# Kernel optimization log

Hardware: AMD Instinct MI355X
Metric: run time of the kernel (lower is better)

Reference implementation:

```python
import jax, jax.numpy as jnp
import numpy as np

STIM_KER_LEN = 50  # length of causal stimulus kernel
K_BASIS = 2        # number of exponential basis functions in history kernel


def setup_inputs() -> dict:
    key = jax.random.key(0)
    T, NTR = 8192, 1024
    k0, k1, k2 = jax.random.split(key, 3)
    t = jnp.arange(T, dtype=jnp.float32)                    # uniform grid, dt = 1.0
    stim = jax.random.normal(k0, (T,), jnp.float32)
    rand = jax.random.uniform(k1, (T, NTR), jnp.float32)    # per-step uniforms (torch.rand in loop)
    # learned parameters
    bias = jnp.array([-4.0], jnp.float32)                   # nn.Parameter bias
    k_stim = jax.random.normal(k2, (STIM_KER_LEN,), jnp.float32) * 0.1  # stim kernel weights
    hist_w = jnp.array([-5.0, 1.0], jnp.float32)            # exponential basis coefficients
    hist_tau = jnp.array([5.0, 20.0], jnp.float32)          # exponential basis time constants
    return dict(t=t, stim=stim, rand=rand, bias=bias, k_stim=k_stim,
                hist_w=hist_w, hist_tau=hist_tau)


def reference(t, stim, rand, bias, k_stim, hist_w, hist_tau):
    dt = t[1] - t[0]
    T = t.shape[0]
    ntr = rand.shape[1]
    # stim_kernel(stim, dt): causal convolution scaled by dt, then shift_tensor(..., 1, fill=0)
    stim_conv = jnp.convolve(stim, k_stim)[:T] * dt                       # (T,)
    stim_conv = jnp.concatenate([jnp.zeros((1,), stim.dtype), stim_conv[:-1]])
    # history kernel: ker(s) = sum_k hist_w[k] * exp(-s / hist_tau[k]), evaluated from 0
    # one step after each spike -> linear recurrence on per-basis state s (K, ntr).
    decay = jnp.exp(-dt / hist_tau)                                        # (K,)

    def step(s, inp):
        sc_j, r_j = inp                       # scalar, (ntr,)
        hist_j = jnp.sum(s, axis=0)           # (ntr,) == hist_conv[j]
        loglam_j = bias[0] + sc_j + hist_j    # (ntr,)
        p_spk = 1.0 - jnp.exp(-jnp.exp(loglam_j) * dt)
        spk_j = p_spk > r_j                   # (ntr,) bool
        s_new = decay[:, None] * s + hist_w[:, None] * spk_j.astype(s.dtype)
        return s_new, (loglam_j, spk_j)

    s0 = jnp.zeros((hist_w.shape[0], ntr), jnp.float32)
    _, (log_lam, mask_spikes) = jax.lax.scan(step, s0, (stim_conv, rand))
    return log_lam, mask_spikes
```

## Files before the change

### kernel.cpp

```cpp
#include <hip/hip_runtime.h>
#include <math.h>

#define T_LEN 8192
#define NTRIALS 1024
#define TN ((size_t)T_LEN * NTRIALS)
#define KLEN 50
#define CHUNK 256
#define NCHUNK (T_LEN / CHUNK)
#define FARW 256
#define NEARW 256
#define WARM (FARW + NEARW)
#define PF 16
#define BAND 1e-4f

__global__ void prep_basc_kernel(const float* __restrict__ t,
                                 const float* __restrict__ stim,
                                 const float* __restrict__ bias,
                                 const float* __restrict__ k_stim,
                                 const float* __restrict__ hist_w,
                                 const float* __restrict__ hist_tau,
                                 double* __restrict__ dparams,
                                 double* __restrict__ basc,
                                 float* __restrict__ bascf) {
  int j = blockIdx.x * blockDim.x + threadIdx.x;
  if (j >= T_LEN) return;
  double dt = (double)t[1] - (double)t[0];
  if (j == 0) {
    dparams[0] = exp(-dt / (double)hist_tau[0]);
    dparams[1] = exp(-dt / (double)hist_tau[1]);
    dparams[2] = (double)hist_w[0];
    dparams[3] = (double)hist_w[1];
    dparams[4] = dt;
    basc[0] = (double)bias[0];
    bascf[0] = (float)(double)bias[0];
    return;
  }
  int n = j - 1;
  int mmax = n < (KLEN - 1) ? n : (KLEN - 1);
  double acc = 0.0;
  for (int m = 0; m <= mmax; ++m)
    acc += (double)k_stim[m] * (double)stim[n - m];
  double v = (double)bias[0] + dt * acc;
  basc[j] = v;
  bascf[j] = (float)v;
}

__global__ void prep_thr32_kernel(const float* __restrict__ rnd,
                                  const float* __restrict__ bascf,
                                  const double* __restrict__ dparams,
                                  float* __restrict__ thr32) {
  size_t m = ((size_t)blockIdx.x * blockDim.x + threadIdx.x) * 4;
  float dtf = (float)dparams[4];
  float4 r4 = *reinterpret_cast<const float4*>(rnd + m);
  float b = bascf[m >> 10];
  float4 o;
  o.x = logf(-log1pf(-r4.x) / dtf) - b;
  o.y = logf(-log1pf(-r4.y) / dtf) - b;
  o.z = logf(-log1pf(-r4.z) / dtf) - b;
  o.w = logf(-log1pf(-r4.w) / dtf) - b;
  *reinterpret_cast<float4*>(thr32 + m) = o;
}

__device__ __noinline__ bool decide64(const float* __restrict__ rnd,
                                      const double* __restrict__ basc,
                                      double dt, int j, int i, double h) {
  double r = (double)rnd[(size_t)j * NTRIALS + i];
  double t = log(-log1p(-r) / dt) - basc[j];
  return h > t;
}

__global__ __launch_bounds__(64, 1) void spec_scan2_kernel(
    const float* __restrict__ thr, const float* __restrict__ rnd,
    const double* __restrict__ basc, const float* __restrict__ bascf,
    const double* __restrict__ dparams, float* __restrict__ out) {
  const int tid = threadIdx.x;
  const int tb  = blockIdx.x & 15;
  const int c   = blockIdx.x >> 4;
  const int i   = tb * 64 + tid;
  const double d0 = dparams[0], d1 = dparams[1];
  const double w0 = dparams[2], w1 = dparams[3];
  const double dt = dparams[4];
  const float d0f = (float)d0, d1f = (float)d1;
  const float w0f = (float)w0, w1f = (float)w1;

  const int jstart = c * CHUNK;
  const int nw    = jstart < WARM ? jstart : WARM;
  const int jw    = jstart - nw;
  const int nearn = nw < NEARW ? nw : NEARW;
  const int farn  = nw - nearn;
  const int j1    = jw + farn;

  const float* __restrict__ p = thr + i;
  float bufA[PF], bufB[PF];
#pragma unroll
  for (int k = 0; k < PF; ++k) bufA[k] = p[(size_t)(jw + k) * NTRIALS];
  __builtin_amdgcn_sched_barrier(0);

  float a0 = 0.0f, a1 = 0.0f;
  for (int q = 0; q < farn; q += 2 * PF) {
    const int j0 = jw + q;
#pragma unroll
    for (int k = 0; k < PF; ++k) bufB[k] = p[(size_t)(j0 + PF + k) * NTRIALS];
    __builtin_amdgcn_sched_barrier(0);
#pragma unroll
    for (int k = 0; k < PF; ++k) {
      float h = a0 + a1;
      bool s = h > bufA[k];
      a0 = fmaf(d0f, a0, s ? w0f : 0.0f);
      a1 = fmaf(d1f, a1, s ? w1f : 0.0f);
    }
    __builtin_amdgcn_sched_barrier(0);
#pragma unroll
    for (int k = 0; k < PF; ++k) bufA[k] = p[(size_t)(j0 + 2 * PF + k) * NTRIALS];
    __builtin_amdgcn_sched_barrier(0);
#pragma unroll
    for (int k = 0; k < PF; ++k) {
      float h = a0 + a1;
      bool s = h > bufB[k];
      a0 = fmaf(d0f, a0, s ? w0f : 0.0f);
      a1 = fmaf(d1f, a1, s ? w1f : 0.0f);
    }
    __builtin_amdgcn_sched_barrier(0);
  }

  double s0 = (double)a0, s1 = (double)a1;
  for (int q = 0; q < nearn; q += 2 * PF) {
    const int j0 = j1 + q;
#pragma unroll
    for (int k = 0; k < PF; ++k) bufB[k] = p[(size_t)(j0 + PF + k) * NTRIALS];
    __builtin_amdgcn_sched_barrier(0);
#pragma unroll
    for (int k = 0; k < PF; ++k) {
      double h = s0 + s1;
      float d = (float)h - bufA[k];
      bool s = d > 0.0f;
      if (__builtin_expect(fabsf(d) < BAND, 0))
        s = decide64(rnd, basc, dt, j0 + k, i, h);
      s0 = fma(d0, s0, s ? w0 : 0.0);
      s1 = fma(d1, s1, s ? w1 : 0.0);
    }
    __builtin_amdgcn_sched_barrier(0);
#pragma unroll
    for (int k = 0; k < PF; ++k) bufA[k] = p[(size_t)(j0 + 2 * PF + k) * NTRIALS];
    __builtin_amdgcn_sched_barrier(0);
#pragma unroll
    for (int k = 0; k < PF; ++k) {
      double h = s0 + s1;
      float d = (float)h - bufB[k];
      bool s = d > 0.0f;
      if (__builtin_expect(fabsf(d) < BAND, 0))
        s = decide64(rnd, basc, dt, j0 + PF + k, i, h);
      s0 = fma(d0, s0, s ? w0 : 0.0);
      s1 = fma(d1, s1, s ? w1 : 0.0);
    }
    __builtin_amdgcn_sched_barrier(0);
  }

  float* __restrict__ po_ll = out + (size_t)jstart * NTRIALS + i;
  float* __restrict__ po_mk = po_ll + TN;
  for (int q = 0; q < CHUNK; q += 2 * PF) {
    const int j0 = jstart + q;
#pragma unroll
    for (int k = 0; k < PF; ++k) bufB[k] = p[(size_t)(j0 + PF + k) * NTRIALS];
    __builtin_amdgcn_sched_barrier(0);
#pragma unroll
    for (int k = 0; k < PF; ++k) {
      double h = s0 + s1;
      float d = (float)h - bufA[k];
      bool s = d > 0.0f;
      if (__builtin_expect(fabsf(d) < BAND, 0))
        s = decide64(rnd, basc, dt, j0 + k, i, h);
      po_ll[(size_t)(q + k) * NTRIALS] = (float)h + bascf[j0 + k];
      po_mk[(size_t)(q + k) * NTRIALS] = s ? 1.0f : 0.0f;
      s0 = fma(d0, s0, s ? w0 : 0.0);
      s1 = fma(d1, s1, s ? w1 : 0.0);
    }
    __builtin_amdgcn_sched_barrier(0);
    if (q + 2 * PF < CHUNK) {
#pragma unroll
      for (int k = 0; k < PF; ++k)
        bufA[k] = p[(size_t)(j0 + 2 * PF + k) * NTRIALS];
    }
    __builtin_amdgcn_sched_barrier(0);
#pragma unroll
    for (int k = 0; k < PF; ++k) {
      double h = s0 + s1;
      float d = (float)h - bufB[k];
      bool s = d > 0.0f;
      if (__builtin_expect(fabsf(d) < BAND, 0))
        s = decide64(rnd, basc, dt, j0 + PF + k, i, h);
      po_ll[(size_t)(q + PF + k) * NTRIALS] = (float)h + bascf[j0 + PF + k];
      po_mk[(size_t)(q + PF + k) * NTRIALS] = s ? 1.0f : 0.0f;
      s0 = fma(d0, s0, s ? w0 : 0.0);
      s1 = fma(d1, s1, s ? w1 : 0.0);
    }
    __builtin_amdgcn_sched_barrier(0);
  }
}

__global__ __launch_bounds__(64, 1) void glm_scan_inline_kernel(
    const float* __restrict__ rnd, const double* __restrict__ basc,
    const double* __restrict__ dparams, float* __restrict__ out) {
  const int i = blockIdx.x * 64 + threadIdx.x;
  const double d0 = dparams[0], d1 = dparams[1];
  const double w0 = dparams[2], w1 = dparams[3];
  const double dt = dparams[4];
  double s0 = 0.0, s1 = 0.0;
  float* __restrict__ out_ll = out;
  float* __restrict__ out_mk = out + TN;
  for (int j = 0; j < T_LEN; ++j) {
    double r = (double)rnd[(size_t)j * NTRIALS + i];
    double th = log(-log1p(-r) / dt) - basc[j];
    double hist = s0 + s1;
    bool spk = hist > th;
    out_ll[(size_t)j * NTRIALS + i] = (float)(basc[j] + hist);
    out_mk[(size_t)j * NTRIALS + i] = spk ? 1.0f : 0.0f;
    s0 = fma(d0, s0, spk ? w0 : 0.0);
    s1 = fma(d1, s1, spk ? w1 : 0.0);
  }
}

extern "C" void kernel_launch(void* const* d_in, const int* in_sizes, int n_in,
                              void* d_out, int out_size, void* d_ws, size_t ws_size,
                              hipStream_t stream) {
  const float* t        = (const float*)d_in[0];
  const float* stim     = (const float*)d_in[1];
  const float* rnd      = (const float*)d_in[2];
  const float* bias     = (const float*)d_in[3];
  const float* k_stim   = (const float*)d_in[4];
  const float* hist_w   = (const float*)d_in[5];
  const float* hist_tau = (const float*)d_in[6];
  float* out = (float*)d_out;

  char* ws = (char*)d_ws;
  const size_t off_bascf = 64;
  const size_t off_basc  = off_bascf + (size_t)T_LEN * 4;
  const size_t off_thr   = off_basc + (size_t)T_LEN * 8;
  const size_t need_full = off_thr + TN * 4;
  const size_t need_min  = off_thr;

  double* dparams = (double*)ws;
  float*  bascf   = (float*)(ws + off_bascf);
  double* basc    = (double*)(ws + off_basc);
  float*  thr32   = (float*)(ws + off_thr);

  prep_basc_kernel<<<(T_LEN + 255) / 256, 256, 0, stream>>>(
      t, stim, bias, k_stim, hist_w, hist_tau, dparams, basc, bascf);

  if (ws_size >= need_full) {
    prep_thr32_kernel<<<(int)(TN / 4 / 256), 256, 0, stream>>>(
        rnd, bascf, dparams, thr32);
    spec_scan2_kernel<<<NCHUNK * 16, 64, 0, stream>>>(
        thr32, rnd, basc, bascf, dparams, out);
  } else if (ws_size >= need_min) {
    glm_scan_inline_kernel<<<NTRIALS / 64, 64, 0, stream>>>(rnd, basc, dparams, out);
  }
}
```

Measured before the change: 96.34 us.

## Fuse threshold computation into chunked scan, halve chunk size, deepen prefetch

Removes the separate prep kernel that turned the uniforms into log-space thresholds, which wrote and then reread a full T×NTR float array. The scan now computes each threshold inline from the raw random value, using a precomputed log(dt). Chunk size is halved to 128 to launch twice as many blocks, and the prefetch depth is doubled to 32. The cost is more transcendental work inside the scan, including on the warm-up steps, which are repeated for every chunk, so redundant warm-up work relative to useful output grows.

```diff
diff --git a/kernel.cpp b/kernel.cpp
--- a/kernel.cpp
+++ b/kernel.cpp
@@ -5,12 +5,12 @@
 #define NTRIALS 1024
 #define TN ((size_t)T_LEN * NTRIALS)
 #define KLEN 50
-#define CHUNK 256
+#define CHUNK 128
 #define NCHUNK (T_LEN / CHUNK)
 #define FARW 256
 #define NEARW 256
 #define WARM (FARW + NEARW)
-#define PF 16
+#define PF 32
 #define BAND 1e-4f
 
 __global__ void prep_basc_kernel(const float* __restrict__ t,
@@ -31,6 +31,7 @@
     dparams[2] = (double)hist_w[0];
     dparams[3] = (double)hist_w[1];
     dparams[4] = dt;
+    dparams[5] = log(dt);
     basc[0] = (double)bias[0];
     bascf[0] = (float)(double)bias[0];
     return;
@@ -45,34 +46,16 @@
   bascf[j] = (float)v;
 }
 
-__global__ void prep_thr32_kernel(const float* __restrict__ rnd,
-                                  const float* __restrict__ bascf,
-                                  const double* __restrict__ dparams,
-                                  float* __restrict__ thr32) {
-  size_t m = ((size_t)blockIdx.x * blockDim.x + threadIdx.x) * 4;
-  float dtf = (float)dparams[4];
-  float4 r4 = *reinterpret_cast<const float4*>(rnd + m);
-  float b = bascf[m >> 10];
-  float4 o;
-  o.x = logf(-log1pf(-r4.x) / dtf) - b;
-  o.y = logf(-log1pf(-r4.y) / dtf) - b;
-  o.z = logf(-log1pf(-r4.z) / dtf) - b;
-  o.w = logf(-log1pf(-r4.w) / dtf) - b;
-  *reinterpret_cast<float4*>(thr32 + m) = o;
-}
-
-__device__ __noinline__ bool decide64(const float* __restrict__ rnd,
-                                      const double* __restrict__ basc,
-                                      double dt, int j, int i, double h) {
-  double r = (double)rnd[(size_t)j * NTRIALS + i];
-  double t = log(-log1p(-r) / dt) - basc[j];
-  return h > t;
-}
-
-__global__ __launch_bounds__(64, 1) void spec_scan2_kernel(
-    const float* __restrict__ thr, const float* __restrict__ rnd,
-    const double* __restrict__ basc, const float* __restrict__ bascf,
-    const double* __restrict__ dparams, float* __restrict__ out) {
+__device__ __noinline__ bool decide64r(float r, const double* __restrict__ basc,
+                                       double dt, int j, double h) {
+  double th = log(-log1p(-(double)r) / dt) - basc[j];
+  return h > th;
+}
+
+__global__ __launch_bounds__(64, 1) void fused_scan_kernel(
+    const float* __restrict__ rnd, const double* __restrict__ basc,
+    const float* __restrict__ bascf, const double* __restrict__ dparams,
+    float* __restrict__ out) {
   const int tid = threadIdx.x;
   const int tb  = blockIdx.x & 15;
   const int c   = blockIdx.x >> 4;
@@ -82,6 +65,7 @@
   const double dt = dparams[4];
   const float d0f = (float)d0, d1f = (float)d1;
   const float w0f = (float)w0, w1f = (float)w1;
+  const float ldtf = (float)dparams[5];
 
   const int jstart = c * CHUNK;
   const int nw    = jstart < WARM ? jstart : WARM;
@@ -90,7 +74,7 @@
   const int farn  = nw - nearn;
   const int j1    = jw + farn;
 
-  const float* __restrict__ p = thr + i;
+  const float* __restrict__ p = rnd + i;
   float bufA[PF], bufB[PF];
 #pragma unroll
   for (int k = 0; k < PF; ++k) bufA[k] = p[(size_t)(jw + k) * NTRIALS];
@@ -104,8 +88,9 @@
     __builtin_amdgcn_sched_barrier(0);
 #pragma unroll
     for (int k = 0; k < PF; ++k) {
+      float th = logf(-log1pf(-bufA[k])) - ldtf - bascf[j0 + k];
       float h = a0 + a1;
-      bool s = h > bufA[k];
+      bool s = h > th;
       a0 = fmaf(d0f, a0, s ? w0f : 0.0f);
       a1 = fmaf(d1f, a1, s ? w1f : 0.0f);
     }
@@ -115,8 +100,9 @@
     __builtin_amdgcn_sched_barrier(0);
 #pragma unroll
     for (int k = 0; k < PF; ++k) {
+      float th = logf(-log1pf(-bufB[k])) - ldtf - bascf[j0 + PF + k];
       float h = a0 + a1;
-      bool s = h > bufB[k];
+      bool s = h > th;
       a0 = fmaf(d0f, a0, s ? w0f : 0.0f);
       a1 = fmaf(d1f, a1, s ? w1f : 0.0f);
     }
@@ -131,11 +117,13 @@
     __builtin_amdgcn_sched_barrier(0);
 #pragma unroll
     for (int k = 0; k < PF; ++k) {
-      double h = s0 + s1;
-      float d = (float)h - bufA[k];
-      bool s = d > 0.0f;
-      if (__builtin_expect(fabsf(d) < BAND, 0))
-        s = decide64(rnd, basc, dt, j0 + k, i, h);
+      float r = bufA[k];
+      float th = logf(-log1pf(-r)) - ldtf - bascf[j0 + k];
+      double h = s0 + s1;
+      float d = (float)h - th;
+      bool s = d > 0.0f;
+      if (__builtin_expect(fabsf(d) < BAND, 0))
+        s = decide64r(r, basc, dt, j0 + k, h);
       s0 = fma(d0, s0, s ? w0 : 0.0);
       s1 = fma(d1, s1, s ? w1 : 0.0);
     }
@@ -145,11 +133,13 @@
     __builtin_amdgcn_sched_barrier(0);
 #pragma unroll
     for (int k = 0; k < PF; ++k) {
-      double h = s0 + s1;
-      float d = (float)h - bufB[k];
-      bool s = d > 0.0f;
-      if (__builtin_expect(fabsf(d) < BAND, 0))
-        s = decide64(rnd, basc, dt, j0 + PF + k, i, h);
+      float r = bufB[k];
+      float th = logf(-log1pf(-r)) - ldtf - bascf[j0 + PF + k];
+      double h = s0 + s1;
+      float d = (float)h - th;
+      bool s = d > 0.0f;
+      if (__builtin_expect(fabsf(d) < BAND, 0))
+        s = decide64r(r, basc, dt, j0 + PF + k, h);
       s0 = fma(d0, s0, s ? w0 : 0.0);
       s1 = fma(d1, s1, s ? w1 : 0.0);
     }
@@ -165,12 +155,15 @@
     __builtin_amdgcn_sched_barrier(0);
 #pragma unroll
     for (int k = 0; k < PF; ++k) {
-      double h = s0 + s1;
-      float d = (float)h - bufA[k];
-      bool s = d > 0.0f;
-      if (__builtin_expect(fabsf(d) < BAND, 0))
-        s = decide64(rnd, basc, dt, j0 + k, i, h);
-      po_ll[(size_t)(q + k) * NTRIALS] = (float)h + bascf[j0 + k];
+      float r = bufA[k];
+      float bf = bascf[j0 + k];
+      float th = logf(-log1pf(-r)) - ldtf - bf;
+      double h = s0 + s1;
+      float d = (float)h - th;
+      bool s = d > 0.0f;
+      if (__builtin_expect(fabsf(d) < BAND, 0))
+        s = decide64r(r, basc, dt, j0 + k, h);
+      po_ll[(size_t)(q + k) * NTRIALS] = (float)h + bf;
       po_mk[(size_t)(q + k) * NTRIALS] = s ? 1.0f : 0.0f;
       s0 = fma(d0, s0, s ? w0 : 0.0);
       s1 = fma(d1, s1, s ? w1 : 0.0);
@@ -184,12 +177,15 @@
     __builtin_amdgcn_sched_barrier(0);
 #pragma unroll
     for (int k = 0; k < PF; ++k) {
-      double h = s0 + s1;
-      float d = (float)h - bufB[k];
-      bool s = d > 0.0f;
-      if (__builtin_expect(fabsf(d) < BAND, 0))
-        s = decide64(rnd, basc, dt, j0 + PF + k, i, h);
-      po_ll[(size_t)(q + PF + k) * NTRIALS] = (float)h + bascf[j0 + PF + k];
+      float r = bufB[k];
+      float bf = bascf[j0 + PF + k];
+      float th = logf(-log1pf(-r)) - ldtf - bf;
+      double h = s0 + s1;
+      float d = (float)h - th;
+      bool s = d > 0.0f;
+      if (__builtin_expect(fabsf(d) < BAND, 0))
+        s = decide64r(r, basc, dt, j0 + PF + k, h);
+      po_ll[(size_t)(q + PF + k) * NTRIALS] = (float)h + bf;
       po_mk[(size_t)(q + PF + k) * NTRIALS] = s ? 1.0f : 0.0f;
       s0 = fma(d0, s0, s ? w0 : 0.0);
       s1 = fma(d1, s1, s ? w1 : 0.0);
@@ -235,24 +231,20 @@
   char* ws = (char*)d_ws;
   const size_t off_bascf = 64;
   const size_t off_basc  = off_bascf + (size_t)T_LEN * 4;
-  const size_t off_thr   = off_basc + (size_t)T_LEN * 8;
-  const size_t need_full = off_thr + TN * 4;
-  const size_t need_min  = off_thr;
+  const size_t need      = off_basc + (size_t)T_LEN * 8;
 
   double* dparams = (double*)ws;
   float*  bascf   = (float*)(ws + off_bascf);
   double* basc    = (double*)(ws + off_basc);
-  float*  thr32   = (float*)(ws + off_thr);
 
   prep_basc_kernel<<<(T_LEN + 255) / 256, 256, 0, stream>>>(
       t, stim, bias, k_stim, hist_w, hist_tau, dparams, basc, bascf);
 
-  if (ws_size >= need_full) {
-    prep_thr32_kernel<<<(int)(TN / 4 / 256), 256, 0, stream>>>(
-        rnd, bascf, dparams, thr32);
-    spec_scan2_kernel<<<NCHUNK * 16, 64, 0, stream>>>(
-        thr32, rnd, basc, bascf, dparams, out);
-  } else if (ws_size >= need_min) {
+  if (ws_size >= need) {
+    fused_scan_kernel<<<NCHUNK * 16, 64, 0, stream>>>(
+        rnd, basc, bascf, dparams, out);
+  }
+  else {
     glm_scan_inline_kernel<<<NTRIALS / 64, 64, 0, stream>>>(rnd, basc, dparams, out);
   }
 }
```

After: 217.1 us. 125% more time.
